# Kernel tuning notes

Hardware: AMD Instinct MI355X
Metric: run time of the kernel (lower is better)

## Reference

```python
import jax, jax.numpy as jnp
import numpy as np

D_MODEL = 1024
N_HEADS = 16
D_FF = 4096
LN_EPS = 1e-5


def _linear_params(key, d_in, d_out):
    kw, kb = jax.random.split(key)
    bound = 1.0 / np.sqrt(d_in)
    W = jax.random.uniform(kw, (d_out, d_in), jnp.float32, -bound, bound)
    b = jax.random.uniform(kb, (d_out,), jnp.float32, -bound, bound)
    return W, b


def setup_inputs() -> dict:
    key = jax.random.key(0)
    ks = jax.random.split(key, 8)
    x = jax.random.normal(ks[0], (2, 2048, D_MODEL), jnp.float32)
    Wq, bq = _linear_params(ks[1], D_MODEL, D_MODEL)
    Wk, bk = _linear_params(ks[2], D_MODEL, D_MODEL)
    Wv, bv = _linear_params(ks[3], D_MODEL, D_MODEL)
    Wo, bo = _linear_params(ks[4], D_MODEL, D_MODEL)
    W1, b1 = _linear_params(ks[5], D_MODEL, D_FF)
    W2, b2 = _linear_params(ks[6], D_FF, D_MODEL)
    ln1_g = jnp.ones((D_MODEL,), jnp.float32)
    ln1_b = jnp.zeros((D_MODEL,), jnp.float32)
    ln2_g = jnp.ones((D_MODEL,), jnp.float32)
    ln2_b = jnp.zeros((D_MODEL,), jnp.float32)
    return dict(x=x, Wq=Wq, bq=bq, Wk=Wk, bk=bk, Wv=Wv, bv=bv, Wo=Wo, bo=bo,
                ln1_g=ln1_g, ln1_b=ln1_b, W1=W1, b1=b1, W2=W2, b2=b2,
                ln2_g=ln2_g, ln2_b=ln2_b)


def _layernorm(x, g, b):
    mu = jnp.mean(x, axis=-1, keepdims=True)
    var = jnp.mean(jnp.square(x - mu), axis=-1, keepdims=True)
    return (x - mu) * jax.lax.rsqrt(var + LN_EPS) * g + b


def _lin(x, W, b):
    return jnp.einsum('bsd,ed->bse', x, W) + b


def _attn(x, Wq, bq, Wk, bk, Wv, bv, Wo, bo):
    B, S, _ = x.shape
    d_head = D_MODEL // N_HEADS
    scale = d_head ** -0.5
    split = lambda t: t.reshape(B, S, N_HEADS, d_head).transpose(0, 2, 1, 3)
    q = split(_lin(x, Wq, bq))  # b h s d
    k = split(_lin(x, Wk, bk))
    v = split(_lin(x, Wv, bv))
    scores = jnp.einsum('bhqd,bhkd->bhqk', q, k) * scale
    attn = jax.nn.softmax(scores, axis=-1)
    out = jnp.einsum('bhqk,bhkd->bhqd', attn, v)
    out = out.transpose(0, 2, 1, 3).reshape(B, S, D_MODEL)
    return _lin(out, Wo, bo)


def reference(x, Wq, bq, Wk, bk, Wv, bv, Wo, bo, ln1_g, ln1_b, W1, b1, W2, b2, ln2_g, ln2_b):
    x = x + _attn(_layernorm(x, ln1_g, ln1_b), Wq, bq, Wk, bk, Wv, bv, Wo, bo)
    h = _layernorm(x, ln2_g, ln2_b)
    h = _lin(h, W1, b1)
    h = jax.nn.gelu(h, approximate=False)
    h = _lin(h, W2, b2)
    return x + h
```

## Files before the change

### kernel.cpp

```cpp
#include <hip/hip_runtime.h>
#include <hip/hip_bf16.h>
#include <stdint.h>

#define DM 1024
#define DFF 4096
#define NH 16
#define DH 64
#define SEQ 2048
#define MROWS 4096

typedef unsigned short u16;
typedef __attribute__((ext_vector_type(8))) short bf16x8;
typedef __attribute__((ext_vector_type(4))) float f32x4;
typedef __attribute__((ext_vector_type(16))) float f32x16;
typedef __attribute__((ext_vector_type(4))) unsigned short u16x4;

__device__ __forceinline__ u16 f2b(float f) {
  union { float f; uint32_t u; } v; v.f = f;
  uint32_t r = v.u + 0x7FFFu + ((v.u >> 16) & 1u);
  return (u16)(r >> 16);
}

__device__ __forceinline__ u16 f2bn(float f) {
  __hip_bfloat16 h = __float2bfloat16(f);
  return *reinterpret_cast<u16*>(&h);
}

__device__ __forceinline__ uint32_t pk2(float lo, float hi) {
  return (uint32_t)f2bn(lo) | ((uint32_t)f2bn(hi) << 16);
}

__device__ __forceinline__ void gl_lds16(const void* g, void* l) {
  __builtin_amdgcn_global_load_lds(
      (const __attribute__((address_space(1))) uint32_t*)g,
      (__attribute__((address_space(3))) uint32_t*)l, 16, 0, 0);
}

struct CvtArgs { const float* src[6]; u16* dst[6]; int n4[6]; };

__global__ void cvt_kernel(CvtArgs a) {
  const int stride = gridDim.x * blockDim.x;
  const int t0 = blockIdx.x * blockDim.x + threadIdx.x;
  for (int i = 0; i < 6; ++i) {
    const float4* s = (const float4*)a.src[i];
    u16x4* d = (u16x4*)a.dst[i];
    const int n = a.n4[i];
    for (int idx = t0; idx < n; idx += stride) {
      float4 v = s[idx];
      u16x4 o;
      o[0] = f2b(v.x); o[1] = f2b(v.y); o[2] = f2b(v.z); o[3] = f2b(v.w);
      d[idx] = o;
    }
  }
}

__global__ __launch_bounds__(256)
void ln_kernel(const float* __restrict__ x, const float* __restrict__ g,
               const float* __restrict__ be, u16* __restrict__ out) {
  const int row = blockIdx.x;
  const int tid = threadIdx.x;
  const float4 v = ((const float4*)(x + (size_t)row * DM))[tid];
  float s  = v.x + v.y + v.z + v.w;
  float s2 = v.x * v.x + v.y * v.y + v.z * v.z + v.w * v.w;
  #pragma unroll
  for (int m = 1; m < 64; m <<= 1) {
    s  += __shfl_xor(s,  m, 64);
    s2 += __shfl_xor(s2, m, 64);
  }
  __shared__ float red[8];
  const int w = tid >> 6, lane = tid & 63;
  if (lane == 0) { red[w] = s; red[4 + w] = s2; }
  __syncthreads();
  s  = red[0] + red[1] + red[2] + red[3];
  s2 = red[4] + red[5] + red[6] + red[7];
  const float mu  = s * (1.0f / DM);
  const float var = s2 * (1.0f / DM) - mu * mu;
  const float rstd = rsqrtf(var + 1e-5f);
  const float4 gv = ((const float4*)g)[tid];
  const float4 bv = ((const float4*)be)[tid];
  u16x4 o;
  o[0] = f2b((v.x - mu) * rstd * gv.x + bv.x);
  o[1] = f2b((v.y - mu) * rstd * gv.y + bv.y);
  o[2] = f2b((v.z - mu) * rstd * gv.z + bv.z);
  o[3] = f2b((v.w - mu) * rstd * gv.w + bv.w);
  ((u16x4*)(out + (size_t)row * DM))[tid] = o;
}

__global__ __launch_bounds__(256)
void combine_kernel(const float4* __restrict__ p0, const float4* __restrict__ p1,
                    const float4* __restrict__ bias, const float4* __restrict__ resid,
                    float4* __restrict__ out, int total4, int colmask4) {
  for (int i = blockIdx.x * 256 + threadIdx.x; i < total4; i += gridDim.x * 256) {
    float4 a = p0[i], b = p1[i], bs = bias[i & colmask4], rr = resid[i];
    float4 o;
    o.x = a.x + b.x + bs.x + rr.x;
    o.y = a.y + b.y + bs.y + rr.y;
    o.z = a.z + b.z + bs.z + rr.z;
    o.w = a.w + b.w + bs.w + rr.w;
    out[i] = o;
  }
}

__global__ __launch_bounds__(256)
void combine_ln_kernel(const float4* __restrict__ p0, const float4* __restrict__ p1,
                       const float4* __restrict__ bias, const float4* __restrict__ resid,
                       float4* __restrict__ xout,
                       const float* __restrict__ g, const float* __restrict__ be,
                       u16* __restrict__ nout) {
  const int row = blockIdx.x;
  const int tid = threadIdx.x;
  const int i = row * (DM / 4) + tid;
  const float4 a = p0[i], b = p1[i], bs = bias[tid], rr = resid[i];
  float4 v;
  v.x = a.x + b.x + bs.x + rr.x;
  v.y = a.y + b.y + bs.y + rr.y;
  v.z = a.z + b.z + bs.z + rr.z;
  v.w = a.w + b.w + bs.w + rr.w;
  xout[i] = v;
  float s  = v.x + v.y + v.z + v.w;
  float s2 = v.x * v.x + v.y * v.y + v.z * v.z + v.w * v.w;
  #pragma unroll
  for (int m = 1; m < 64; m <<= 1) {
    s  += __shfl_xor(s,  m, 64);
    s2 += __shfl_xor(s2, m, 64);
  }
  __shared__ float red[8];
  const int w = tid >> 6, lane = tid & 63;
  if (lane == 0) { red[w] = s; red[4 + w] = s2; }
  __syncthreads();
  s  = red[0] + red[1] + red[2] + red[3];
  s2 = red[4] + red[5] + red[6] + red[7];
  const float mu  = s * (1.0f / DM);
  const float var = s2 * (1.0f / DM) - mu * mu;
  const float rstd = rsqrtf(var + 1e-5f);
  const float4 gv = ((const float4*)g)[tid];
  const float4 bv = ((const float4*)be)[tid];
  u16x4 o;
  o[0] = f2b((v.x - mu) * rstd * gv.x + bv.x);
  o[1] = f2b((v.y - mu) * rstd * gv.y + bv.y);
  o[2] = f2b((v.z - mu) * rstd * gv.z + bv.z);
  o[3] = f2b((v.w - mu) * rstd * gv.w + bv.w);
  ((u16x4*)(nout + (size_t)row * DM))[tid] = o;
}

struct GemmPtrs { const u16* W[3]; const float* bias[3]; void* out[3];
                  const float* resid; int vtrans; };

template<int EPI>
__global__ __launch_bounds__(256)
void gemm_bt(const u16* __restrict__ A, GemmPtrs p, int M, int N,
             int Kstride, int Kchunk) {
  __shared__ __align__(16) u16 As[3][128 * 32];
  __shared__ __align__(16) u16 Bs[3][128 * 32];
  const u16* __restrict__ Wm = p.W[blockIdx.z];
  const float* __restrict__ bias = p.bias[blockIdx.z];
  void* outv = p.out[blockIdx.z];
  const float* resid = p.resid;

  const int tid = threadIdx.x;
  const int lane = tid & 63;
  const int w = tid >> 6;
  const int brow = blockIdx.y * 128;
  const int bcol = blockIdx.x * 128;
  const int wr = (w >> 1) * 64, wc = (w & 1) * 64;
  const int koff = (EPI == 3) ? blockIdx.z * Kchunk : 0;

  f32x4 acc[4][4] = {};

  const int srow = tid >> 2;
  const int sc = (((tid & 3) ^ ((tid >> 3) & 3))) * 8;
  const int ldso = w * 512;

  const int nt = Kchunk >> 5;

  auto stage = [&](int t) {
    const int rs = t % 3;
    const int k0 = koff + t * 32;
    gl_lds16(&A [(size_t)(brow + srow) * Kstride + k0 + sc],      &As[rs][ldso]);
    gl_lds16(&A [(size_t)(brow + 64 + srow) * Kstride + k0 + sc], &As[rs][2048 + ldso]);
    gl_lds16(&Wm[(size_t)(bcol + srow) * Kstride + k0 + sc],      &Bs[rs][ldso]);
    gl_lds16(&Wm[(size_t)(bcol + 64 + srow) * Kstride + k0 + sc], &Bs[rs][2048 + ldso]);
  };

  stage(0);
  if (nt > 1) stage(1);

  for (int t = 0; t < nt; ++t) {
    if (t + 1 < nt) asm volatile("s_waitcnt vmcnt(4) lgkmcnt(0)" ::: "memory");
    else            asm volatile("s_waitcnt vmcnt(0) lgkmcnt(0)" ::: "memory");
    __builtin_amdgcn_s_barrier();
    __builtin_amdgcn_sched_barrier(0);
    if (t + 2 < nt) stage(t + 2);

    const int rs = t % 3;
    bf16x8 a[4], b[4];
    #pragma unroll
    for (int f = 0; f < 4; ++f) {
      const int ra = wr + f * 16 + (lane & 15);
      a[f] = *(const bf16x8*)&As[rs][ra * 32 + ((lane >> 4) ^ ((ra >> 1) & 3)) * 8];
      const int rb = wc + f * 16 + (lane & 15);
      b[f] = *(const bf16x8*)&Bs[rs][rb * 32 + ((lane >> 4) ^ ((rb >> 1) & 3)) * 8];
    }
    #pragma unroll
    for (int fr = 0; fr < 4; ++fr)
      #pragma unroll
      for (int fc = 0; fc < 4; ++fc)
        acc[fr][fc] = __builtin_amdgcn_mfma_f32_16x16x32_bf16(a[fr], b[fc], acc[fr][fc], 0, 0, 0);
  }

  const int orow0 = brow + wr + (lane >> 4) * 4;
  const int ocol0 = bcol + wc + (lane & 15);

  if (EPI == 0 && p.vtrans && blockIdx.z == 2) {
    #pragma unroll
    for (int fr = 0; fr < 4; ++fr) {
      const int row0 = orow0 + fr * 16;
      const int bq = row0 >> 11, s0 = row0 & (SEQ - 1);
      #pragma unroll
      for (int fc = 0; fc < 4; ++fc) {
        const int col = ocol0 + fc * 16;
        const float bvv = bias[col];
        u16x4 o;
        #pragma unroll
        for (int r = 0; r < 4; ++r) o[r] = f2b(acc[fr][fc][r] + bvv);
        *(u16x4*)((u16*)outv + (size_t)(bq * DM + col) * SEQ + s0) = o;
      }
    }
    return;
  }

  const float oscale = (EPI == 0 && p.vtrans && blockIdx.z == 0) ? 0.125f : 1.0f;

  #pragma unroll
  for (int fr = 0; fr < 4; ++fr) {
    #pragma unroll
    for (int fc = 0; fc < 4; ++fc) {
      const int col = ocol0 + fc * 16;
      const float bvv = (EPI == 3) ? 0.0f : bias[col];
      #pragma unroll
      for (int r = 0; r < 4; ++r) {
        const int row = orow0 + fr * 16 + r;
        const size_t idx = (size_t)row * N + col;
        float v = acc[fr][fc][r] + bvv;
        if (EPI == 0) {
          ((u16*)outv)[idx] = f2b(v * oscale);
        } else if (EPI == 1) {
          float ge = 0.5f * v * (1.0f + erff(v * 0.70710678118654752f));
          ((u16*)outv)[idx] = f2b(ge);
        } else if (EPI == 2) {
          ((float*)outv)[idx] = v + resid[idx];
        } else {
          ((float*)outv)[idx] = v;
        }
      }
    }
  }
}

__global__ __launch_bounds__(128, 4)
void attn_kernel(const u16* __restrict__ Q, const u16* __restrict__ K,
                 const u16* __restrict__ Vt, float* __restrict__ Opart,
                 float2* __restrict__ ML) {
  __shared__ __align__(16) u16 Ks[64 * 64];
  __shared__ __align__(16) u16 Vts[64 * 64];
  const int tid = threadIdx.x, lane = tid & 63, w = tid >> 6;
  const int bh = blockIdx.y, b = bh >> 4, h = bh & 15;
  const int kvh = blockIdx.z;
  const int q0 = blockIdx.x * 64 + w * 32;
  const size_t base = (size_t)b * SEQ * DM + (size_t)h * DH;
  const size_t vbase = (size_t)(b * DM + h * DH) * SEQ;
  float* __restrict__ Op = Opart + (size_t)kvh * MROWS * DM;
  float2* __restrict__ mlp = ML + (size_t)kvh * 2 * NH * SEQ;

  const int l31 = lane & 31, hi = lane >> 5, l7 = l31 & 7;

  bf16x8 qf[4];
  {
    const size_t qrow = base + (size_t)(q0 + l31) * DM;
    #pragma unroll
    for (int dt = 0; dt < 4; ++dt)
      qf[dt] = *(const bf16x8*)&Q[qrow + dt * 16 + hi * 8];
  }

  f32x16 oacc[2] = {};
  float mq = -1e30f, lq = 0.0f;

  for (int kt = kvh * (SEQ / 128); kt < (kvh + 1) * (SEQ / 128); ++kt) {
    #pragma unroll
    for (int i = 0; i < 4; ++i) {
      const int r0 = w * 32 + i * 8;
      const int row = r0 + (lane >> 3);
      const int ch = ((lane & 7) ^ (row & 7)) * 8;
      gl_lds16(&K[base + (size_t)(kt * 64 + row) * DM + ch], &Ks[r0 * 64]);
      gl_lds16(&Vt[vbase + (size_t)row * SEQ + kt * 64 + ch], &Vts[r0 * 64]);
    }
    __syncthreads();

    #pragma unroll
    for (int sub = 0; sub < 2; ++sub) {
      f32x16 sacc = {};
      __builtin_amdgcn_s_setprio(1);
      #pragma unroll
      for (int dt = 0; dt < 4; ++dt) {
        bf16x8 kf = *(const bf16x8*)&Ks[(sub * 32 + l31) * 64 + (((dt << 1) | hi) ^ l7) * 8];
        sacc = __builtin_amdgcn_mfma_f32_32x32x16_bf16(kf, qf[dt], sacc, 0, 0, 0);
      }
      __builtin_amdgcn_s_setprio(0);

      float tm = sacc[0];
      #pragma unroll
      for (int r = 1; r < 16; ++r) tm = fmaxf(tm, sacc[r]);
      tm = fmaxf(tm, __shfl_xor(tm, 32, 64));

      if (__any(tm > mq + 8.0f)) {
        const float mnew = fmaxf(mq, tm);
        const float fs = __expf(mq - mnew);
        mq = mnew;
        lq *= fs;
        #pragma unroll
        for (int r = 0; r < 16; ++r) {
          const float fsr = __shfl(fs, (r & 3) + 8 * (r >> 2) + 4 * hi, 64);
          oacc[0][r] *= fsr;
          oacc[1][r] *= fsr;
        }
      }

      uint32_t wd[2][4];
      float ps = 0.0f;
      #pragma unroll
      for (int half = 0; half < 2; ++half) {
        float p[8];
        #pragma unroll
        for (int j = 0; j < 8; ++j) {
          p[j] = __expf(sacc[half * 8 + j] - mq);
          ps += p[j];
        }
        const uint32_t a = pk2(p[0], p[1]), c = pk2(p[2], p[3]);
        const uint32_t bb = pk2(p[4], p[5]), d = pk2(p[6], p[7]);
        const uint32_t xa = (uint32_t)__shfl_xor((int)a, 32, 64);
        const uint32_t xb = (uint32_t)__shfl_xor((int)bb, 32, 64);
        const uint32_t xc = (uint32_t)__shfl_xor((int)c, 32, 64);
        const uint32_t xd = (uint32_t)__shfl_xor((int)d, 32, 64);
        wd[half][0] = hi ? xb : a;
        wd[half][1] = hi ? xd : c;
        wd[half][2] = hi ? bb : xa;
        wd[half][3] = hi ? d : xc;
      }
      lq += ps;
      bf16x8 pa0, pa1;
      #pragma unroll
      for (int j = 0; j < 4; ++j) {
        ((uint32_t*)&pa0)[j] = wd[0][j];
        ((uint32_t*)&pa1)[j] = wd[1][j];
      }

      __builtin_amdgcn_s_setprio(1);
      #pragma unroll
      for (int dt = 0; dt < 2; ++dt) {
        #pragma unroll
        for (int ks = 0; ks < 2; ++ks) {
          bf16x8 vf = *(const bf16x8*)&Vts[(dt * 32 + l31) * 64 +
                                           (((sub << 2) | (ks << 1) | hi) ^ l7) * 8];
          oacc[dt] = __builtin_amdgcn_mfma_f32_32x32x16_bf16(ks ? pa1 : pa0, vf, oacc[dt], 0, 0, 0);
        }
      }
      __builtin_amdgcn_s_setprio(0);
    }
    __syncthreads();
  }

  const float ltot = lq + __shfl_xor(lq, 32, 64);
  #pragma unroll
  for (int r = 0; r < 16; ++r) {
    const int crow = (r & 3) + 8 * (r >> 2) + 4 * hi;
    const size_t orow = base + (size_t)(q0 + crow) * DM;
    Op[orow + l31]      = oacc[0][r];
    Op[orow + 32 + l31] = oacc[1][r];
  }
  if (hi == 0) mlp[(size_t)bh * SEQ + q0 + l31] = make_float2(mq, ltot);
}

__global__ __launch_bounds__(256)
void attn_merge(const float4* __restrict__ Op0, const float4* __restrict__ Op1,
                const float2* __restrict__ ML, u16* __restrict__ ao) {
  const int row = blockIdx.x, tid = threadIdx.x;
  const int idx4 = row * (DM / 4) + tid;
  const int bh = ((row >> 11) << 4) | (tid >> 4);
  const int s = row & (SEQ - 1);
  const float2 a = ML[(size_t)bh * SEQ + s];
  const float2 c = ML[(size_t)(2 * NH) * SEQ + (size_t)bh * SEQ + s];
  const float m = fmaxf(a.x, c.x);
  const float f0 = __expf(a.x - m), f1 = __expf(c.x - m);
  const float inv = 1.0f / (a.y * f0 + c.y * f1);
  const float4 o0 = Op0[idx4], o1 = Op1[idx4];
  u16x4 o;
  o[0] = f2bn((o0.x * f0 + o1.x * f1) * inv);
  o[1] = f2bn((o0.y * f0 + o1.y * f1) * inv);
  o[2] = f2bn((o0.z * f0 + o1.z * f1) * inv);
  o[3] = f2bn((o0.w * f0 + o1.w * f1) * inv);
  ((u16x4*)ao)[idx4] = o;
}

extern "C" void kernel_launch(void* const* d_in, const int* in_sizes, int n_in,
                              void* d_out, int out_size, void* d_ws, size_t ws_size,
                              hipStream_t stream) {
  const float* x    = (const float*)d_in[0];
  const float* Wq   = (const float*)d_in[1];
  const float* bq   = (const float*)d_in[2];
  const float* Wk   = (const float*)d_in[3];
  const float* bk   = (const float*)d_in[4];
  const float* Wv   = (const float*)d_in[5];
  const float* bv   = (const float*)d_in[6];
  const float* Wo   = (const float*)d_in[7];
  const float* bo   = (const float*)d_in[8];
  const float* ln1g = (const float*)d_in[9];
  const float* ln1b = (const float*)d_in[10];
  const float* W1   = (const float*)d_in[11];
  const float* b1   = (const float*)d_in[12];
  const float* W2   = (const float*)d_in[13];
  const float* b2   = (const float*)d_in[14];
  const float* ln2g = (const float*)d_in[15];
  const float* ln2b = (const float*)d_in[16];
  float* out = (float*)d_out;

  char* wsb = (char*)d_ws;
  size_t off = 0;
  auto alloc = [&](size_t bytes) -> char* {
    char* pp = wsb + off;
    off += (bytes + 255) & ~(size_t)255;
    return pp;
  };
  u16* Wq_b = (u16*)alloc((size_t)DM * DM * 2);
  u16* Wk_b = (u16*)alloc((size_t)DM * DM * 2);
  u16* Wv_b = (u16*)alloc((size_t)DM * DM * 2);
  u16* Wo_b = (u16*)alloc((size_t)DM * DM * 2);
  u16* W1_b = (u16*)alloc((size_t)DFF * DM * 2);
  u16* W2_b = (u16*)alloc((size_t)DM * DFF * 2);
  u16* xn   = (u16*)alloc((size_t)MROWS * DM * 2);
  u16* qb   = (u16*)alloc((size_t)MROWS * DM * 2);
  u16* kb   = (u16*)alloc((size_t)MROWS * DM * 2);
  u16* vt   = (u16*)alloc((size_t)MROWS * DM * 2);
  u16* ao   = (u16*)alloc((size_t)MROWS * DM * 2);
  u16* h1   = (u16*)alloc((size_t)MROWS * DFF * 2);
  float2* ml = (float2*)alloc((size_t)2 * 2 * NH * SEQ * sizeof(float2));

  float* pA = (float*)xn;
  float* pB = (float*)kb;
  float* attnOp = (float*)h1;

  CvtArgs ca;
  ca.src[0] = Wq; ca.dst[0] = Wq_b; ca.n4[0] = DM * DM / 4;
  ca.src[1] = Wk; ca.dst[1] = Wk_b; ca.n4[1] = DM * DM / 4;
  ca.src[2] = Wv; ca.dst[2] = Wv_b; ca.n4[2] = DM * DM / 4;
  ca.src[3] = Wo; ca.dst[3] = Wo_b; ca.n4[3] = DM * DM / 4;
  ca.src[4] = W1; ca.dst[4] = W1_b; ca.n4[4] = DFF * DM / 4;
  ca.src[5] = W2; ca.dst[5] = W2_b; ca.n4[5] = DM * DFF / 4;
  cvt_kernel<<<2048, 256, 0, stream>>>(ca);

  ln_kernel<<<MROWS, 256, 0, stream>>>(x, ln1g, ln1b, xn);

  GemmPtrs pq = {};
  pq.W[0] = Wq_b; pq.W[1] = Wk_b; pq.W[2] = Wv_b;
  pq.bias[0] = bq; pq.bias[1] = bk; pq.bias[2] = bv;
  pq.out[0] = qb; pq.out[1] = kb; pq.out[2] = vt;
  pq.vtrans = 1;
  gemm_bt<0><<<dim3(DM / 128, MROWS / 128, 3), 256, 0, stream>>>(xn, pq, MROWS, DM, DM, DM);

  attn_kernel<<<dim3(SEQ / 64, 2 * NH, 2), 128, 0, stream>>>(qb, kb, vt, attnOp, ml);
  attn_merge<<<MROWS, 256, 0, stream>>>((const float4*)attnOp,
                                        (const float4*)(attnOp + (size_t)MROWS * DM),
                                        (const float2*)ml, ao);

  GemmPtrs po = {};
  po.W[0] = Wo_b; po.W[1] = Wo_b;
  po.bias[0] = bo; po.bias[1] = bo;
  po.out[0] = pA; po.out[1] = pB;
  gemm_bt<3><<<dim3(DM / 128, MROWS / 128, 2), 256, 0, stream>>>(ao, po, MROWS, DM, DM, DM / 2);
  combine_ln_kernel<<<MROWS, 256, 0, stream>>>((const float4*)pA, (const float4*)pB,
                                               (const float4*)bo, (const float4*)x,
                                               (float4*)out, ln2g, ln2b, ao);

  GemmPtrs p1 = {};
  p1.W[0] = W1_b; p1.bias[0] = b1; p1.out[0] = h1;
  gemm_bt<1><<<dim3(DFF / 128, MROWS / 128, 1), 256, 0, stream>>>(ao, p1, MROWS, DFF, DM, DM);

  GemmPtrs p2 = {};
  p2.W[0] = W2_b; p2.W[1] = W2_b;
  p2.bias[0] = b2; p2.bias[1] = b2;
  p2.out[0] = pA; p2.out[1] = pB;
  gemm_bt<3><<<dim3(DM / 128, MROWS / 128, 2), 256, 0, stream>>>(h1, p2, MROWS, DM, DFF, DFF / 2);
  combine_kernel<<<2048, 256, 0, stream>>>((const float4*)pA, (const float4*)pB,
                                           (const float4*)b2, (const float4*)out,
                                           (float4*)out, MROWS * DM / 4, DM / 4 - 1);
}
```

Before: 301.5 us.

## Split-K four ways for output and FFN2 GEMMs, double-buffer LDS

The Wo and W2 GEMMs move from 2-way to 4-way split-K, with new four-partial combine kernels (one fused with LayerNorm). The FFN2 path uses two extra fp32 workspace buffers and falls back to 2-way when the workspace is too small. The GEMM kernel drops from a triple-buffered LDS pipeline with explicit waitcnt control to double buffering with __syncthreads and a launch_bounds occupancy hint of 4. The goal is to fill more CUs on the small-N GEMMs and raise occupancy, at the cost of extra fp32 partial-sum traffic and a pipeline that hides less latency.

```diff
diff --git a/kernel.cpp b/kernel.cpp
--- a/kernel.cpp
+++ b/kernel.cpp
@@ -102,20 +102,39 @@
 }
 
 __global__ __launch_bounds__(256)
-void combine_ln_kernel(const float4* __restrict__ p0, const float4* __restrict__ p1,
-                       const float4* __restrict__ bias, const float4* __restrict__ resid,
-                       float4* __restrict__ xout,
-                       const float* __restrict__ g, const float* __restrict__ be,
-                       u16* __restrict__ nout) {
+void combine4_kernel(const float4* __restrict__ p0, const float4* __restrict__ p1,
+                     const float4* __restrict__ p2, const float4* __restrict__ p3,
+                     const float4* __restrict__ bias, const float4* __restrict__ resid,
+                     float4* __restrict__ out, int total4, int colmask4) {
+  for (int i = blockIdx.x * 256 + threadIdx.x; i < total4; i += gridDim.x * 256) {
+    float4 a = p0[i], b = p1[i], c = p2[i], d = p3[i];
+    float4 bs = bias[i & colmask4], rr = resid[i];
+    float4 o;
+    o.x = (a.x + b.x) + (c.x + d.x) + bs.x + rr.x;
+    o.y = (a.y + b.y) + (c.y + d.y) + bs.y + rr.y;
+    o.z = (a.z + b.z) + (c.z + d.z) + bs.z + rr.z;
+    o.w = (a.w + b.w) + (c.w + d.w) + bs.w + rr.w;
+    out[i] = o;
+  }
+}
+
+__global__ __launch_bounds__(256)
+void combine4_ln_kernel(const float4* __restrict__ p0, const float4* __restrict__ p1,
+                        const float4* __restrict__ p2, const float4* __restrict__ p3,
+                        const float4* __restrict__ bias, const float4* __restrict__ resid,
+                        float4* __restrict__ xout,
+                        const float* __restrict__ g, const float* __restrict__ be,
+                        u16* __restrict__ nout) {
   const int row = blockIdx.x;
   const int tid = threadIdx.x;
   const int i = row * (DM / 4) + tid;
-  const float4 a = p0[i], b = p1[i], bs = bias[tid], rr = resid[i];
+  const float4 a = p0[i], b = p1[i], c = p2[i], d = p3[i];
+  const float4 bs = bias[tid], rr = resid[i];
   float4 v;
-  v.x = a.x + b.x + bs.x + rr.x;
-  v.y = a.y + b.y + bs.y + rr.y;
-  v.z = a.z + b.z + bs.z + rr.z;
-  v.w = a.w + b.w + bs.w + rr.w;
+  v.x = (a.x + b.x) + (c.x + d.x) + bs.x + rr.x;
+  v.y = (a.y + b.y) + (c.y + d.y) + bs.y + rr.y;
+  v.z = (a.z + b.z) + (c.z + d.z) + bs.z + rr.z;
+  v.w = (a.w + b.w) + (c.w + d.w) + bs.w + rr.w;
   xout[i] = v;
   float s  = v.x + v.y + v.z + v.w;
   float s2 = v.x * v.x + v.y * v.y + v.z * v.z + v.w * v.w;
@@ -143,15 +162,15 @@
   ((u16x4*)(nout + (size_t)row * DM))[tid] = o;
 }
 
-struct GemmPtrs { const u16* W[3]; const float* bias[3]; void* out[3];
+struct GemmPtrs { const u16* W[4]; const float* bias[4]; void* out[4];
                   const float* resid; int vtrans; };
 
 template<int EPI>
-__global__ __launch_bounds__(256)
+__global__ __launch_bounds__(256, 4)
 void gemm_bt(const u16* __restrict__ A, GemmPtrs p, int M, int N,
              int Kstride, int Kchunk) {
-  __shared__ __align__(16) u16 As[3][128 * 32];
-  __shared__ __align__(16) u16 Bs[3][128 * 32];
+  __shared__ __align__(16) u16 As[2][128 * 32];
+  __shared__ __align__(16) u16 Bs[2][128 * 32];
   const u16* __restrict__ Wm = p.W[blockIdx.z];
   const float* __restrict__ bias = p.bias[blockIdx.z];
   void* outv = p.out[blockIdx.z];
@@ -168,44 +187,40 @@
   f32x4 acc[4][4] = {};
 
   const int srow = tid >> 2;
-  const int sc = (((tid & 3) ^ ((tid >> 3) & 3))) * 8;
+  const int sc = ((tid & 3) ^ ((tid >> 3) & 3)) * 8;
   const int ldso = w * 512;
 
   const int nt = Kchunk >> 5;
 
   auto stage = [&](int t) {
-    const int rs = t % 3;
+    const int sl = t & 1;
     const int k0 = koff + t * 32;
-    gl_lds16(&A [(size_t)(brow + srow) * Kstride + k0 + sc],      &As[rs][ldso]);
-    gl_lds16(&A [(size_t)(brow + 64 + srow) * Kstride + k0 + sc], &As[rs][2048 + ldso]);
-    gl_lds16(&Wm[(size_t)(bcol + srow) * Kstride + k0 + sc],      &Bs[rs][ldso]);
-    gl_lds16(&Wm[(size_t)(bcol + 64 + srow) * Kstride + k0 + sc], &Bs[rs][2048 + ldso]);
+    gl_lds16(&A [(size_t)(brow + srow) * Kstride + k0 + sc],      &As[sl][ldso]);
+    gl_lds16(&A [(size_t)(brow + 64 + srow) * Kstride + k0 + sc], &As[sl][2048 + ldso]);
+    gl_lds16(&Wm[(size_t)(bcol + srow) * Kstride + k0 + sc],      &Bs[sl][ldso]);
+    gl_lds16(&Wm[(size_t)(bcol + 64 + srow) * Kstride + k0 + sc], &Bs[sl][2048 + ldso]);
   };
 
   stage(0);
-  if (nt > 1) stage(1);
+  __syncthreads();
 
   for (int t = 0; t < nt; ++t) {
-    if (t + 1 < nt) asm volatile("s_waitcnt vmcnt(4) lgkmcnt(0)" ::: "memory");
-    else            asm volatile("s_waitcnt vmcnt(0) lgkmcnt(0)" ::: "memory");
-    __builtin_amdgcn_s_barrier();
-    __builtin_amdgcn_sched_barrier(0);
-    if (t + 2 < nt) stage(t + 2);
-
-    const int rs = t % 3;
+    if (t + 1 < nt) stage(t + 1);
+    const int sl = t & 1;
     bf16x8 a[4], b[4];
     #pragma unroll
     for (int f = 0; f < 4; ++f) {
       const int ra = wr + f * 16 + (lane & 15);
-      a[f] = *(const bf16x8*)&As[rs][ra * 32 + ((lane >> 4) ^ ((ra >> 1) & 3)) * 8];
+      a[f] = *(const bf16x8*)&As[sl][ra * 32 + ((lane >> 4) ^ ((ra >> 1) & 3)) * 8];
       const int rb = wc + f * 16 + (lane & 15);
-      b[f] = *(const bf16x8*)&Bs[rs][rb * 32 + ((lane >> 4) ^ ((rb >> 1) & 3)) * 8];
+      b[f] = *(const bf16x8*)&Bs[sl][rb * 32 + ((lane >> 4) ^ ((rb >> 1) & 3)) * 8];
     }
     #pragma unroll
     for (int fr = 0; fr < 4; ++fr)
       #pragma unroll
       for (int fc = 0; fc < 4; ++fc)
         acc[fr][fc] = __builtin_amdgcn_mfma_f32_16x16x32_bf16(a[fr], b[fc], acc[fr][fc], 0, 0, 0);
+    __syncthreads();
   }
 
   const int orow0 = brow + wr + (lane >> 4) * 4;
@@ -443,9 +458,14 @@
   u16* ao   = (u16*)alloc((size_t)MROWS * DM * 2);
   u16* h1   = (u16*)alloc((size_t)MROWS * DFF * 2);
   float2* ml = (float2*)alloc((size_t)2 * 2 * NH * SEQ * sizeof(float2));
+  float* pX = (float*)alloc((size_t)MROWS * DM * 4);
+  float* pY = (float*)alloc((size_t)MROWS * DM * 4);
+  const bool ffn2x4 = (off <= ws_size);
 
   float* pA = (float*)xn;
   float* pB = (float*)kb;
+  float* pC = (float*)h1;
+  float* pD = (float*)((char*)h1 + (size_t)MROWS * DM * 4);
   float* attnOp = (float*)h1;
 
   CvtArgs ca;
@@ -472,24 +492,37 @@
                                         (const float2*)ml, ao);
 
   GemmPtrs po = {};
-  po.W[0] = Wo_b; po.W[1] = Wo_b;
-  po.bias[0] = bo; po.bias[1] = bo;
-  po.out[0] = pA; po.out[1] = pB;
-  gemm_bt<3><<<dim3(DM / 128, MROWS / 128, 2), 256, 0, stream>>>(ao, po, MROWS, DM, DM, DM / 2);
-  combine_ln_kernel<<<MROWS, 256, 0, stream>>>((const float4*)pA, (const float4*)pB,
-                                               (const float4*)bo, (const float4*)x,
-                                               (float4*)out, ln2g, ln2b, ao);
+  po.W[0] = po.W[1] = po.W[2] = po.W[3] = Wo_b;
+  po.bias[0] = po.bias[1] = po.bias[2] = po.bias[3] = bo;
+  po.out[0] = pA; po.out[1] = pB; po.out[2] = pC; po.out[3] = pD;
+  gemm_bt<3><<<dim3(DM / 128, MROWS / 128, 4), 256, 0, stream>>>(ao, po, MROWS, DM, DM, DM / 4);
+  combine4_ln_kernel<<<MROWS, 256, 0, stream>>>((const float4*)pA, (const float4*)pB,
+                                                (const float4*)pC, (const float4*)pD,
+                                                (const float4*)bo, (const float4*)x,
+                                                (float4*)out, ln2g, ln2b, ao);
 
   GemmPtrs p1 = {};
   p1.W[0] = W1_b; p1.bias[0] = b1; p1.out[0] = h1;
   gemm_bt<1><<<dim3(DFF / 128, MROWS / 128, 1), 256, 0, stream>>>(ao, p1, MROWS, DFF, DM, DM);
 
-  GemmPtrs p2 = {};
-  p2.W[0] = W2_b; p2.W[1] = W2_b;
-  p2.bias[0] = b2; p2.bias[1] = b2;
-  p2.out[0] = pA; p2.out[1] = pB;
-  gemm_bt<3><<<dim3(DM / 128, MROWS / 128, 2), 256, 0, stream>>>(h1, p2, MROWS, DM, DFF, DFF / 2);
-  combine_kernel<<<2048, 256, 0, stream>>>((const float4*)pA, (const float4*)pB,
-                                           (const float4*)b2, (const float4*)out,
-                                           (float4*)out, MROWS * DM / 4, DM / 4 - 1);
-}
+  if (ffn2x4) {
+    GemmPtrs p2 = {};
+    p2.W[0] = p2.W[1] = p2.W[2] = p2.W[3] = W2_b;
+    p2.bias[0] = p2.bias[1] = p2.bias[2] = p2.bias[3] = b2;
+    p2.out[0] = pA; p2.out[1] = pB; p2.out[2] = pX; p2.out[3] = pY;
+    gemm_bt<3><<<dim3(DM / 128, MROWS / 128, 4), 256, 0, stream>>>(h1, p2, MROWS, DM, DFF, DFF / 4);
+    combine4_kernel<<<2048, 256, 0, stream>>>((const float4*)pA, (const float4*)pB,
+                                              (const float4*)pX, (const float4*)pY,
+                                              (const float4*)b2, (const float4*)out,
+                                              (float4*)out, MROWS * DM / 4, DM / 4 - 1);
+  } else {
+    GemmPtrs p2 = {};
+    p2.W[0] = p2.W[1] = W2_b;
+    p2.bias[0] = p2.bias[1] = b2;
+    p2.out[0] = pA; p2.out[1] = pB;
+    gemm_bt<3><<<dim3(DM / 128, MROWS / 128, 2), 256, 0, stream>>>(h1, p2, MROWS, DM, DFF, DFF / 2);
+    combine_kernel<<<2048, 256, 0, stream>>>((const float4*)pA, (const float4*)pB,
+                                             (const float4*)b2, (const float4*)out,
+                                             (float4*)out, MROWS * DM / 4, DM / 4 - 1);
+  }
+}
```

Measured after the change: 290.6 us. 1.04x faster.
